# Kernel tuning notes

Measured on AMD Instinct MI355X. Metric: run time of the kernel, lower is better.

## Reference

```python
import jax, jax.numpy as jnp
import numpy as np

CODEBOOK_DIM = 12          # log2(codebook_size)
CODEBOOK_SIZE = 4096
DIM = 512
INV_TEMPERATURE = 100.0
CODEBOOK_SCALE = 1.0
DIVERSITY_GAMMA = 1.0
ENTROPY_LOSS_WEIGHT = 0.1
EPS = 1e-5


def setup_inputs() -> dict:
    key = jax.random.key(0)
    k_x, k_wi, k_wo = jax.random.split(key, 3)
    x = jax.random.normal(k_x, (4, 4096, DIM), dtype=jnp.float32)
    # nn.Linear weights: (out_features, in_features)
    w_in = jax.random.normal(k_wi, (CODEBOOK_DIM, DIM), dtype=jnp.float32) * 0.02
    b_in = jnp.zeros((CODEBOOK_DIM,), dtype=jnp.float32)
    w_out = jax.random.normal(k_wo, (DIM, CODEBOOK_DIM), dtype=jnp.float32) * 0.02
    b_out = jnp.zeros((DIM,), dtype=jnp.float32)
    return {"x": x, "w_in": w_in, "b_in": b_in, "w_out": w_out, "b_out": b_out}


def _entropy(prob):
    return (-prob * jnp.log(jnp.clip(prob, EPS))).sum(axis=-1)


def _make_codebook():
    mask = (2 ** jnp.arange(CODEBOOK_DIM - 1, -1, -1)).astype(jnp.int32)  # [d]
    all_codes = jnp.arange(CODEBOOK_SIZE, dtype=jnp.int32)
    bits = ((all_codes[:, None] & mask) != 0).astype(jnp.float32)  # [cs, d]
    codebook = bits * CODEBOOK_SCALE * 2 - CODEBOOK_SCALE  # {-1, +1}
    return mask, codebook


def reference(x, w_in, b_in, w_out, b_out):
    mask, codebook = _make_codebook()

    # project in: [b, n, dim] -> [b, n, d]
    xp = jnp.einsum('bnd,cd->bnc', x, w_in) + b_in  # c == codebook_dim here

    # sign quantization (num_codebooks = 1, so c-dim is implicit)
    quantized = jnp.where(xp > 0, CODEBOOK_SCALE, -CODEBOOK_SCALE).astype(xp.dtype)
    indices = ((quantized > 0).astype(jnp.int32) * mask).sum(axis=-1)  # [b, n]

    # straight-through estimator (training path)
    x_st = xp + jax.lax.stop_gradient(quantized - xp)

    # entropy aux loss over full codebook (frac_per_sample_entropy = 1.0)
    flat = xp.reshape(-1, CODEBOOK_DIM)  # original (pre-quant) input, [bn, d]
    # -distance * inv_temp = 2 * inv_temp * <x, code>
    logits = (2.0 * INV_TEMPERATURE) * (flat @ codebook.T)  # [bn, cs]
    prob = jax.nn.softmax(logits, axis=-1)
    per_sample_entropy = _entropy(prob).mean()
    avg_prob = prob.mean(axis=0)  # [cs]
    codebook_entropy = _entropy(avg_prob)
    entropy_aux_loss = per_sample_entropy - DIVERSITY_GAMMA * codebook_entropy
    aux_loss = entropy_aux_loss * ENTROPY_LOSS_WEIGHT

    # project out: [b, n, d] -> [b, n, dim]
    out = jnp.einsum('bnc,dc->bnd', x_st, w_out) + b_out
    return out, indices, aux_loss
```

## Files before the change

### kernel.cpp

```cpp
#include <hip/hip_runtime.h>
#include <hip/hip_bf16.h>


#define NS    16384
#define NOUT  (NS*512)
#define AUXO  (NOUT+NS)
#define INVT2 200.0f
#define PBLK  256
#define EBLK  256
#define RBLK  64

template <int CTRL>
__device__ inline float dpp_add(float v) {
  int p = __builtin_amdgcn_update_dpp(0, __float_as_int(v), CTRL, 0xF, 0xF, true);
  return v + __int_as_float(p);
}
__device__ inline float rdlane(float v, int lane) {
  return __int_as_float(__builtin_amdgcn_readlane(__float_as_int(v), lane));
}

__global__ __launch_bounds__(512, 2) void k_proj(
    const float* __restrict__ x,
    const float* __restrict__ w_in,  const float* __restrict__ b_in,
    const float* __restrict__ w_out, const float* __restrict__ b_out,
    float* __restrict__ out, float* __restrict__ idx_out,
    float* __restrict__ xp_out) {

  __shared__ float s_wi[6144];
  __shared__ float s_wt[6144];

  const int t = threadIdx.x;

  for (int k = 0; k < 12; ++k) {
    int f  = t + k * 512;
    int kk = f & 3;
    int q  = f >> 2;
    int sub = q & 15, e4 = (q >> 4) & 7, d = q >> 7;
    int e  = sub * 32 + e4 * 4 + kk;
    s_wi[f] = w_in[d * 512 + e];
    s_wt[f] = w_out[t * 12 + k];
  }
  __syncthreads();

  const int wave = t >> 6, lane = t & 63;
  const int g = lane >> 4, sub = lane & 15;

  float bin[12];
  #pragma unroll
  for (int d = 0; d < 12; ++d) bin[d] = b_in[d];

  const int i0 = blockIdx.x * 64 + wave * 8 + g;
  const int i1 = i0 + 4;

  const float4* xr0 = (const float4*)(x + (size_t)i0 * 512 + sub * 32);
  const float4* xr1 = (const float4*)(x + (size_t)i1 * 512 + sub * 32);
  float4 xv0[8], xv1[8];
  #pragma unroll
  for (int e4 = 0; e4 < 8; ++e4) { xv0[e4] = xr0[e4]; xv1[e4] = xr1[e4]; }

  float p0[12], p1[12];
  #pragma unroll
  for (int d = 0; d < 12; ++d) { p0[d] = 0.f; p1[d] = 0.f; }
  #pragma unroll
  for (int e4 = 0; e4 < 8; ++e4) {
    #pragma unroll
    for (int d = 0; d < 12; ++d) {
      float4 w4 = ((const float4*)s_wi)[d * 128 + e4 * 16 + sub];
      p0[d] += xv0[e4].x * w4.x + xv0[e4].y * w4.y + xv0[e4].z * w4.z + xv0[e4].w * w4.w;
      p1[d] += xv1[e4].x * w4.x + xv1[e4].y * w4.y + xv1[e4].z * w4.z + xv1[e4].w * w4.w;
    }
  }
  #pragma unroll
  for (int d = 0; d < 12; ++d) {
    #pragma unroll
    for (int m = 1; m <= 8; m <<= 1) {
      p0[d] += __shfl_xor(p0[d], m, 16);
      p1[d] += __shfl_xor(p1[d], m, 16);
    }
    p0[d] += bin[d];
    p1[d] += bin[d];
  }

  unsigned idx0 = 0u, idx1 = 0u;
  #pragma unroll
  for (int d = 0; d < 12; ++d) {
    idx0 |= (p0[d] > 0.f ? 1u : 0u) << (11 - d);
    idx1 |= (p1[d] > 0.f ? 1u : 0u) << (11 - d);
  }
  if (sub == 0) {
    idx_out[i0] = (float)idx0;
    idx_out[i1] = (float)idx1;
  }

  {
    float4 v0 = make_float4(p0[0], p0[1], p0[2], p0[3]);
    float4 v1 = make_float4(p1[0], p1[1], p1[2], p1[3]);
    if (sub == 1) { v0 = make_float4(p0[4], p0[5], p0[6], p0[7]);
                    v1 = make_float4(p1[4], p1[5], p1[6], p1[7]); }
    if (sub == 2) { v0 = make_float4(p0[8], p0[9], p0[10], p0[11]);
                    v1 = make_float4(p1[8], p1[9], p1[10], p1[11]); }
    if (sub < 3) {
      ((float4*)(xp_out + (size_t)i0 * 12))[sub] = v0;
      ((float4*)(xp_out + (size_t)i1 * 12))[sub] = v1;
    }
  }

  float sg0[12], sg1[12];
  #pragma unroll
  for (int d = 0; d < 12; ++d) {
    sg0[d] = p0[d] > 0.f ? 1.f : -1.f;
    sg1[d] = p1[d] > 0.f ? 1.f : -1.f;
  }
  float4* or0 = (float4*)(out + (size_t)i0 * 512);
  float4* or1 = (float4*)(out + (size_t)i1 * 512);
  #pragma unroll
  for (int e4 = 0; e4 < 8; ++e4) {
    float4 bo = ((const float4*)b_out)[e4 * 16 + sub];
    float4 o0 = bo, o1 = bo;
    #pragma unroll
    for (int d = 0; d < 12; ++d) {
      float4 w4 = ((const float4*)s_wt)[d * 128 + e4 * 16 + sub];
      o0.x += sg0[d] * w4.x; o0.y += sg0[d] * w4.y; o0.z += sg0[d] * w4.z; o0.w += sg0[d] * w4.w;
      o1.x += sg1[d] * w4.x; o1.y += sg1[d] * w4.y; o1.z += sg1[d] * w4.z; o1.w += sg1[d] * w4.w;
    }
    or0[e4 * 16 + sub] = o0;
    or1[e4 * 16 + sub] = o1;
  }
}

__global__ __launch_bounds__(512) void k_ent(
    const float* __restrict__ xp,
    float* __restrict__ P, float* __restrict__ scal) {

  __shared__ float s_phi[64][64];
  __shared__ float s_psi[64][64];
  __shared__ float s_h[8];

  const int t = threadIdx.x;
  const int wave = t >> 6, lane = t & 63;
  const int sbase = blockIdx.x * 64 + wave * 8;

  float hacc = 0.f;
  #pragma unroll 1
  for (int s = 0; s < 8; ++s) {
    const float* xps = xp + (size_t)(sbase + s) * 12;
    float xq[12];
    #pragma unroll
    for (int d = 0; d < 12; ++d) xq[d] = xps[d];

    float hi = 0.f, lo = 0.f, ah = 0.f, al = 0.f;
    #pragma unroll
    for (int d = 0; d < 6; ++d) {
      int bh = (lane >> (5 - d)) & 1;
      hi += bh ? xq[d]     : -xq[d];
      lo += bh ? xq[6 + d] : -xq[6 + d];
      ah += fabsf(xq[d]);
      al += fabsf(xq[6 + d]);
    }
    float lhi = INVT2 * (hi - ah);
    float llo = INVT2 * (lo - al);
    float ehi = __expf(lhi);
    float elo = __expf(llo);

    float Shi = ehi, Slo = elo;
    Shi = dpp_add<0xB1>(Shi);  Slo = dpp_add<0xB1>(Slo);
    Shi = dpp_add<0x4E>(Shi);  Slo = dpp_add<0x4E>(Slo);
    Shi = dpp_add<0x141>(Shi); Slo = dpp_add<0x141>(Slo);
    Shi = dpp_add<0x140>(Shi); Slo = dpp_add<0x140>(Slo);
    {
      float r0 = rdlane(Shi, 0), r1 = rdlane(Shi, 16), r2 = rdlane(Shi, 32), r3 = rdlane(Shi, 48);
      Shi = (r0 + r1) + (r2 + r3);
      float q0 = rdlane(Slo, 0), q1 = rdlane(Slo, 16), q2 = rdlane(Slo, 32), q3 = rdlane(Slo, 48);
      Slo = (q0 + q1) + (q2 + q3);
    }

    float phi = ehi / Shi;
    float psi = elo / Slo;
    float lnShi = __logf(Shi), lnSlo = __logf(Slo);
    hacc += phi * (lhi - lnShi) + psi * (llo - lnSlo);

    s_phi[wave * 8 + s][lane] = phi;
    s_psi[wave * 8 + s][lane] = psi;
  }

  #pragma unroll
  for (int m = 1; m <= 32; m <<= 1) hacc += __shfl_xor(hacc, m);
  if (lane == 0) s_h[wave] = hacc;
  __syncthreads();
  if (t == 0) {
    float hs = 0.f;
    for (int w2 = 0; w2 < 8; ++w2) hs += s_h[w2];
    atomicAdd(&scal[0], hs);
  }

  const int jb = (t >> 5) * 4;
  const int lb = (t & 31) * 2;
  float a00 = 0.f, a01 = 0.f, a10 = 0.f, a11 = 0.f;
  float a20 = 0.f, a21 = 0.f, a30 = 0.f, a31 = 0.f;
  #pragma unroll 4
  for (int s = 0; s < 64; ++s) {
    float4 ph = *(const float4*)&s_phi[s][jb];
    float2 ps = *(const float2*)&s_psi[s][lb];
    a00 += ph.x * ps.x; a01 += ph.x * ps.y;
    a10 += ph.y * ps.x; a11 += ph.y * ps.y;
    a20 += ph.z * ps.x; a21 += ph.z * ps.y;
    a30 += ph.w * ps.x; a31 += ph.w * ps.y;
  }
  float* Pr = P + (size_t)blockIdx.x * 4096;
  *(float2*)&Pr[(jb + 0) * 64 + lb] = make_float2(a00, a01);
  *(float2*)&Pr[(jb + 1) * 64 + lb] = make_float2(a10, a11);
  *(float2*)&Pr[(jb + 2) * 64 + lb] = make_float2(a20, a21);
  *(float2*)&Pr[(jb + 3) * 64 + lb] = make_float2(a30, a31);
}

__global__ __launch_bounds__(256) void k_reduce(const float* __restrict__ P,
                                                float* __restrict__ scal,
                                                float* __restrict__ aux) {
  __shared__ float red[4][64];
  const int t = threadIdx.x;
  const int c = blockIdx.x * 64 + (t & 63);
  const int rg = t >> 6;
  float s = 0.f;
  #pragma unroll 8
  for (int j = 0; j < 64; ++j) s += P[(size_t)(rg * 64 + j) * 4096 + c];
  red[rg][t & 63] = s;
  __syncthreads();
  if (t < 64) {
    float tot = (red[0][t] + red[1][t]) + (red[2][t] + red[3][t]);
    float pb = tot * (1.f / (float)NS);
    float e = pb * __logf(fmaxf(pb, 1e-5f));
    #pragma unroll
    for (int m = 1; m <= 32; m <<= 1) e += __shfl_xor(e, m);
    if (t == 0) {
      atomicAdd(&scal[1], e);
      __threadfence();
      unsigned done = atomicAdd((unsigned*)&scal[2], 1u);
      if (done == RBLK - 1) {
        float E = atomicAdd(&scal[1], 0.f);
        float C = atomicAdd(&scal[0], 0.f);
        float per_sample_entropy = -C * (1.f / (float)NS);
        float codebook_entropy   = -E;
        aux[0] = 0.1f * (per_sample_entropy - codebook_entropy);
      }
    }
  }
}

extern "C" void kernel_launch(void* const* d_in, const int* in_sizes, int n_in,
                              void* d_out, int out_size, void* d_ws, size_t ws_size,
                              hipStream_t stream) {
  const float* x     = (const float*)d_in[0];
  const float* w_in  = (const float*)d_in[1];
  const float* b_in  = (const float*)d_in[2];
  const float* w_out = (const float*)d_in[3];
  const float* b_out = (const float*)d_in[4];
  float* out = (float*)d_out;

  float* P    = (float*)d_ws;
  float* xp   = P + (size_t)EBLK * 4096;
  float* scal = xp + (size_t)NS * 12;

  hipMemsetAsync(scal, 0, 3 * sizeof(float), stream);
  k_proj<<<PBLK, 512, 0, stream>>>(x, w_in, b_in, w_out, b_out,
                                   out, out + NOUT, xp);
  k_ent<<<EBLK, 512, 0, stream>>>(xp, P, scal);
  k_reduce<<<RBLK, 256, 0, stream>>>(P, scal, out + AUXO);
}
```

Before: 116.1 us.

## Fuse projection, entropy, and reduction into one cooperative kernel with grid syncs

Merges the three kernels and the memset into a single cooperative launch. The projected 12-dim vectors now pass through shared memory instead of a global xp buffer, and the final reduction runs after two grid-wide syncs. This removes launch gaps and the xp global round trip. In exchange it adds two grid barriers and uses more shared memory per block, which may limit occupancy. The reduction is also split across 8 row groups.

```diff
diff --git a/kernel.cpp b/kernel.cpp
--- a/kernel.cpp
+++ b/kernel.cpp
@@ -1,13 +1,14 @@
 #include <hip/hip_runtime.h>
-#include <hip/hip_bf16.h>
+#include <hip/hip_cooperative_groups.h>
+
+namespace cg = cooperative_groups;
 
 
 #define NS    16384
 #define NOUT  (NS*512)
 #define AUXO  (NOUT+NS)
 #define INVT2 200.0f
-#define PBLK  256
-#define EBLK  256
+#define NBLK  256
 #define RBLK  64
 
 template <int CTRL>
@@ -19,17 +20,23 @@
   return __int_as_float(__builtin_amdgcn_readlane(__float_as_int(v), lane));
 }
 
-__global__ __launch_bounds__(512, 2) void k_proj(
+__global__ __launch_bounds__(512, 2) void k_all(
     const float* __restrict__ x,
     const float* __restrict__ w_in,  const float* __restrict__ b_in,
     const float* __restrict__ w_out, const float* __restrict__ b_out,
     float* __restrict__ out, float* __restrict__ idx_out,
-    float* __restrict__ xp_out) {
+    float* __restrict__ P, float* __restrict__ scal, float* __restrict__ aux) {
 
   __shared__ float s_wi[6144];
   __shared__ float s_wt[6144];
-
-  const int t = threadIdx.x;
+  __shared__ float s_phi[64][64];
+  __shared__ float s_psi[64][64];
+  __shared__ float s_xp[8][8][12];
+  __shared__ float s_h[8];
+  __shared__ float red[8][64];
+
+  const int t   = threadIdx.x;
+  const int bid = blockIdx.x;
 
   for (int k = 0; k < 12; ++k) {
     int f  = t + k * 512;
@@ -40,6 +47,9 @@
     s_wi[f] = w_in[d * 512 + e];
     s_wt[f] = w_out[t * 12 + k];
   }
+  if (bid == 0 && t == 0) {
+    scal[0] = 0.f; scal[1] = 0.f; ((unsigned*)scal)[2] = 0u;
+  }
   __syncthreads();
 
   const int wave = t >> 6, lane = t & 63;
@@ -49,7 +59,7 @@
   #pragma unroll
   for (int d = 0; d < 12; ++d) bin[d] = b_in[d];
 
-  const int i0 = blockIdx.x * 64 + wave * 8 + g;
+  const int i0 = bid * 64 + wave * 8 + g;
   const int i1 = i0 + 4;
 
   const float4* xr0 = (const float4*)(x + (size_t)i0 * 512 + sub * 32);
@@ -90,18 +100,10 @@
   if (sub == 0) {
     idx_out[i0] = (float)idx0;
     idx_out[i1] = (float)idx1;
-  }
-
-  {
-    float4 v0 = make_float4(p0[0], p0[1], p0[2], p0[3]);
-    float4 v1 = make_float4(p1[0], p1[1], p1[2], p1[3]);
-    if (sub == 1) { v0 = make_float4(p0[4], p0[5], p0[6], p0[7]);
-                    v1 = make_float4(p1[4], p1[5], p1[6], p1[7]); }
-    if (sub == 2) { v0 = make_float4(p0[8], p0[9], p0[10], p0[11]);
-                    v1 = make_float4(p1[8], p1[9], p1[10], p1[11]); }
-    if (sub < 3) {
-      ((float4*)(xp_out + (size_t)i0 * 12))[sub] = v0;
-      ((float4*)(xp_out + (size_t)i1 * 12))[sub] = v1;
+    #pragma unroll
+    for (int d = 0; d < 12; ++d) {
+      s_xp[wave][g][d]     = p0[d];
+      s_xp[wave][4 + g][d] = p1[d];
     }
   }
 
@@ -126,27 +128,13 @@
     or0[e4 * 16 + sub] = o0;
     or1[e4 * 16 + sub] = o1;
   }
-}
-
-__global__ __launch_bounds__(512) void k_ent(
-    const float* __restrict__ xp,
-    float* __restrict__ P, float* __restrict__ scal) {
-
-  __shared__ float s_phi[64][64];
-  __shared__ float s_psi[64][64];
-  __shared__ float s_h[8];
-
-  const int t = threadIdx.x;
-  const int wave = t >> 6, lane = t & 63;
-  const int sbase = blockIdx.x * 64 + wave * 8;
 
   float hacc = 0.f;
   #pragma unroll 1
   for (int s = 0; s < 8; ++s) {
-    const float* xps = xp + (size_t)(sbase + s) * 12;
     float xq[12];
     #pragma unroll
-    for (int d = 0; d < 12; ++d) xq[d] = xps[d];
+    for (int d = 0; d < 12; ++d) xq[d] = s_xp[wave][s][d];
 
     float hi = 0.f, lo = 0.f, ah = 0.f, al = 0.f;
     #pragma unroll
@@ -187,60 +175,64 @@
   for (int m = 1; m <= 32; m <<= 1) hacc += __shfl_xor(hacc, m);
   if (lane == 0) s_h[wave] = hacc;
   __syncthreads();
+
+  float hs = 0.f;
   if (t == 0) {
-    float hs = 0.f;
+    #pragma unroll
     for (int w2 = 0; w2 < 8; ++w2) hs += s_h[w2];
-    atomicAdd(&scal[0], hs);
-  }
-
-  const int jb = (t >> 5) * 4;
-  const int lb = (t & 31) * 2;
-  float a00 = 0.f, a01 = 0.f, a10 = 0.f, a11 = 0.f;
-  float a20 = 0.f, a21 = 0.f, a30 = 0.f, a31 = 0.f;
-  #pragma unroll 4
-  for (int s = 0; s < 64; ++s) {
-    float4 ph = *(const float4*)&s_phi[s][jb];
-    float2 ps = *(const float2*)&s_psi[s][lb];
-    a00 += ph.x * ps.x; a01 += ph.x * ps.y;
-    a10 += ph.y * ps.x; a11 += ph.y * ps.y;
-    a20 += ph.z * ps.x; a21 += ph.z * ps.y;
-    a30 += ph.w * ps.x; a31 += ph.w * ps.y;
-  }
-  float* Pr = P + (size_t)blockIdx.x * 4096;
-  *(float2*)&Pr[(jb + 0) * 64 + lb] = make_float2(a00, a01);
-  *(float2*)&Pr[(jb + 1) * 64 + lb] = make_float2(a10, a11);
-  *(float2*)&Pr[(jb + 2) * 64 + lb] = make_float2(a20, a21);
-  *(float2*)&Pr[(jb + 3) * 64 + lb] = make_float2(a30, a31);
-}
-
-__global__ __launch_bounds__(256) void k_reduce(const float* __restrict__ P,
-                                                float* __restrict__ scal,
-                                                float* __restrict__ aux) {
-  __shared__ float red[4][64];
-  const int t = threadIdx.x;
-  const int c = blockIdx.x * 64 + (t & 63);
-  const int rg = t >> 6;
-  float s = 0.f;
-  #pragma unroll 8
-  for (int j = 0; j < 64; ++j) s += P[(size_t)(rg * 64 + j) * 4096 + c];
-  red[rg][t & 63] = s;
-  __syncthreads();
-  if (t < 64) {
-    float tot = (red[0][t] + red[1][t]) + (red[2][t] + red[3][t]);
-    float pb = tot * (1.f / (float)NS);
-    float e = pb * __logf(fmaxf(pb, 1e-5f));
-    #pragma unroll
-    for (int m = 1; m <= 32; m <<= 1) e += __shfl_xor(e, m);
-    if (t == 0) {
-      atomicAdd(&scal[1], e);
-      __threadfence();
-      unsigned done = atomicAdd((unsigned*)&scal[2], 1u);
-      if (done == RBLK - 1) {
-        float E = atomicAdd(&scal[1], 0.f);
-        float C = atomicAdd(&scal[0], 0.f);
-        float per_sample_entropy = -C * (1.f / (float)NS);
-        float codebook_entropy   = -E;
-        aux[0] = 0.1f * (per_sample_entropy - codebook_entropy);
+  }
+
+  {
+    const int jb = (t >> 5) * 4;
+    const int lb = (t & 31) * 2;
+    float a00 = 0.f, a01 = 0.f, a10 = 0.f, a11 = 0.f;
+    float a20 = 0.f, a21 = 0.f, a30 = 0.f, a31 = 0.f;
+    #pragma unroll 4
+    for (int s = 0; s < 64; ++s) {
+      float4 ph = *(const float4*)&s_phi[s][jb];
+      float2 ps = *(const float2*)&s_psi[s][lb];
+      a00 += ph.x * ps.x; a01 += ph.x * ps.y;
+      a10 += ph.y * ps.x; a11 += ph.y * ps.y;
+      a20 += ph.z * ps.x; a21 += ph.z * ps.y;
+      a30 += ph.w * ps.x; a31 += ph.w * ps.y;
+    }
+    float* Pr = P + (size_t)bid * 4096;
+    *(float2*)&Pr[(jb + 0) * 64 + lb] = make_float2(a00, a01);
+    *(float2*)&Pr[(jb + 1) * 64 + lb] = make_float2(a10, a11);
+    *(float2*)&Pr[(jb + 2) * 64 + lb] = make_float2(a20, a21);
+    *(float2*)&Pr[(jb + 3) * 64 + lb] = make_float2(a30, a31);
+  }
+
+  cg::this_grid().sync();
+  if (t == 0) atomicAdd(&scal[0], hs);
+  cg::this_grid().sync();
+
+  if (bid < RBLK) {
+    const int c  = bid * 64 + (t & 63);
+    const int rg = t >> 6;
+    float s = 0.f;
+    #pragma unroll 8
+    for (int j = 0; j < 32; ++j) s += P[(size_t)(rg * 32 + j) * 4096 + c];
+    red[rg][t & 63] = s;
+    __syncthreads();
+    if (t < 64) {
+      float tot = (((red[0][t] + red[1][t]) + (red[2][t] + red[3][t])) +
+                   ((red[4][t] + red[5][t]) + (red[6][t] + red[7][t])));
+      float pb = tot * (1.f / (float)NS);
+      float e = pb * __logf(fmaxf(pb, 1e-5f));
+      #pragma unroll
+      for (int m = 1; m <= 32; m <<= 1) e += __shfl_xor(e, m);
+      if (t == 0) {
+        atomicAdd(&scal[1], e);
+        __threadfence();
+        unsigned done = atomicAdd((unsigned*)&scal[2], 1u);
+        if (done == RBLK - 1) {
+          float E = atomicAdd(&scal[1], 0.f);
+          float C = atomicAdd(&scal[0], 0.f);
+          float per_sample_entropy = -C * (1.f / (float)NS);
+          float codebook_entropy   = -E;
+          aux[0] = 0.1f * (per_sample_entropy - codebook_entropy);
+        }
       }
     }
   }
@@ -254,15 +246,14 @@
   const float* b_in  = (const float*)d_in[2];
   const float* w_out = (const float*)d_in[3];
   const float* b_out = (const float*)d_in[4];
-  float* out = (float*)d_out;
+  float* out     = (float*)d_out;
+  float* idx_out = out + NOUT;
+  float* aux     = out + AUXO;
 
   float* P    = (float*)d_ws;
-  float* xp   = P + (size_t)EBLK * 4096;
-  float* scal = xp + (size_t)NS * 12;
-
-  hipMemsetAsync(scal, 0, 3 * sizeof(float), stream);
-  k_proj<<<PBLK, 512, 0, stream>>>(x, w_in, b_in, w_out, b_out,
-                                   out, out + NOUT, xp);
-  k_ent<<<EBLK, 512, 0, stream>>>(xp, P, scal);
-  k_reduce<<<RBLK, 256, 0, stream>>>(P, scal, out + AUXO);
-}
+  float* scal = P + (size_t)NBLK * 4096;
+
+  void* args[] = { (void*)&x, (void*)&w_in, (void*)&b_in, (void*)&w_out, (void*)&b_out,
+                   (void*)&out, (void*)&idx_out, (void*)&P, (void*)&scal, (void*)&aux };
+  hipLaunchCooperativeKernel((const void*)k_all, dim3(NBLK), dim3(512), args, 0, stream);
+}
```

New measurement: 179.3 us. +54.4%, slower.
